# Kernel tuning notes

Measured on AMD Instinct MI355X. Metric: run time of the kernel, lower is better.

Reference implementation:

```python
import jax, jax.numpy as jnp
import numpy as np
from jax import lax

BN_EPS = 1e-5
K_TOP = 2


def _conv_bn_relu_pool(x, w, b, g, beta, mean, var):
    # x: [B,C,H,W], w: [O,I,3,3]; SAME conv -> eval BN -> ReLU -> 2x2 maxpool
    y = lax.conv_general_dilated(x, w, (1, 1), 'SAME',
                                 dimension_numbers=('NCHW', 'OIHW', 'NCHW'))
    y = y + b[None, :, None, None]
    inv = g / jnp.sqrt(var + BN_EPS)
    y = (y - mean[None, :, None, None]) * inv[None, :, None, None] + beta[None, :, None, None]
    y = jax.nn.relu(y)
    return lax.reduce_window(y, -jnp.inf, lax.max, (1, 1, 2, 2), (1, 1, 2, 2), 'VALID')


def setup_inputs() -> dict:
    key = jax.random.key(0)
    ks = jax.random.split(key, 12)
    B, F_DIM, H_DIM, OUT, E = 4096, 128, 64, 10, 8
    d = {}
    d['x'] = jax.random.normal(ks[0], (B, 3, 32, 32), dtype=jnp.float32)
    # conv stacks
    def conv_block(k, cin, cout, i):
        kk = jax.random.split(k, 2)
        d[f'conv{i}_w'] = jax.random.normal(kk[0], (cout, cin, 3, 3), dtype=jnp.float32) * (1.0 / np.sqrt(cin * 9))
        d[f'conv{i}_b'] = jnp.zeros((cout,), dtype=jnp.float32)
        d[f'bn{i}_g'] = jnp.ones((cout,), dtype=jnp.float32)
        d[f'bn{i}_b'] = jnp.zeros((cout,), dtype=jnp.float32)
        d[f'bn{i}_m'] = jax.random.normal(kk[1], (cout,), dtype=jnp.float32) * 0.1
        d[f'bn{i}_v'] = jnp.ones((cout,), dtype=jnp.float32)
    conv_block(ks[1], 3, 32, 1)
    conv_block(ks[2], 32, 64, 2)
    conv_block(ks[3], 64, 128, 3)
    # experts (stacked): MLPHead Linear(128,64) -> ReLU -> Linear(64,10)
    d['w1'] = jax.random.normal(ks[4], (E, F_DIM, H_DIM), dtype=jnp.float32) * (1.0 / np.sqrt(F_DIM))
    d['b1'] = jnp.zeros((E, H_DIM), dtype=jnp.float32)
    d['w2'] = jax.random.normal(ks[5], (E, H_DIM, OUT), dtype=jnp.float32) * (1.0 / np.sqrt(H_DIM))
    d['b2'] = jnp.zeros((E, OUT), dtype=jnp.float32)
    # top-k gate: Linear(128, 8)
    d['gate_w'] = jax.random.normal(ks[6], (F_DIM, E), dtype=jnp.float32) * (1.0 / np.sqrt(F_DIM))
    d['gate_b'] = jnp.zeros((E,), dtype=jnp.float32)
    return d


def reference(x, conv1_w, conv1_b, bn1_g, bn1_b, bn1_m, bn1_v,
              conv2_w, conv2_b, bn2_g, bn2_b, bn2_m, bn2_v,
              conv3_w, conv3_b, bn3_g, bn3_b, bn3_m, bn3_v,
              w1, b1, w2, b2, gate_w, gate_b):
    # Backbone: 3x32x32 -> 128 (eval-mode BN, dropout identity)
    h = _conv_bn_relu_pool(x, conv1_w, conv1_b, bn1_g, bn1_b, bn1_m, bn1_v)  # [B,32,16,16]
    h = _conv_bn_relu_pool(h, conv2_w, conv2_b, bn2_g, bn2_b, bn2_m, bn2_v)  # [B,64,8,8]
    h = _conv_bn_relu_pool(h, conv3_w, conv3_b, bn3_g, bn3_b, bn3_m, bn3_v)  # [B,128,4,4]
    feat = jnp.mean(h, axis=(2, 3))  # AdaptiveAvgPool2d(1) + Flatten -> [B,128]

    # Top-k gate: logits -> top-k -> softmax over selected -> scatter to [B,E]
    logits = feat @ gate_w + gate_b                     # [B,E]
    vals, idx = lax.top_k(logits, K_TOP)                # [B,k]
    wk = jax.nn.softmax(vals, axis=-1)                  # [B,k]
    B, E = logits.shape
    weights = jnp.zeros((B, E), dtype=logits.dtype)
    weights = weights.at[jnp.arange(B)[:, None], idx].set(wk)

    # Dense expert MLPs (as in source), gate-weighted sum
    he = jax.nn.relu(jnp.einsum('bf,efh->beh', feat, w1) + b1[None])  # [B,E,H]
    oe = jnp.einsum('beh,eho->beo', he, w2) + b2[None]                # [B,E,O]
    return jnp.einsum('be,beo->bo', weights, oe)                      # [B,O]
```

## Files before the change

### kernel.cpp

```cpp
#include <hip/hip_runtime.h>
#include <math.h>

typedef __attribute__((ext_vector_type(8))) short short8;
typedef __attribute__((ext_vector_type(4))) float f32x4;
#define MFMA __builtin_amdgcn_mfma_f32_16x16x32_bf16

#define BN_EPS 1e-5f

static const size_t W1C2_OFF = 0;
static const size_t W2C2_OFF = 1024;
static const size_t W3C2_OFF = 19456;
static const size_t B1_OFF   = 93184;
static const size_t B2_OFF   = 93216;
static const size_t B3_OFF   = 93280;

__device__ inline unsigned short rneb(float x) {
    unsigned u = __float_as_uint(x);
    return (unsigned short)((u + 0x7FFFu + ((u >> 16) & 1u)) >> 16);
}
__device__ inline float b2f(unsigned short h) {
    return __uint_as_float(((unsigned)h) << 16);
}

__global__ __launch_bounds__(256) void k_prep(
    const float* __restrict__ c1w, const float* __restrict__ c2w, const float* __restrict__ c3w,
    const float* __restrict__ c1b, const float* __restrict__ g1, const float* __restrict__ be1,
    const float* __restrict__ m1, const float* __restrict__ v1,
    const float* __restrict__ c2b, const float* __restrict__ g2, const float* __restrict__ be2,
    const float* __restrict__ m2, const float* __restrict__ v2,
    const float* __restrict__ c3b, const float* __restrict__ g3, const float* __restrict__ be3,
    const float* __restrict__ m3, const float* __restrict__ v3,
    unsigned short* __restrict__ w1c2, unsigned short* __restrict__ w2c2,
    unsigned short* __restrict__ w3c2,
    float* __restrict__ b1c, float* __restrict__ b2c, float* __restrict__ b3c)
{
    int i = blockIdx.x * 256 + threadIdx.x;
    if (i < 2048) {
        int e = i & 7, p = (i >> 3) & 1, kc = (i >> 4) & 3, ol = (i >> 6) & 15, n = i >> 10;
        int o = n * 16 + ol, k = kc * 8 + e;
        float s = g1[o] * rsqrtf(v1[o] + BN_EPS);
        float wv = (k < 27) ? c1w[o * 27 + k] * s : 0.f;
        unsigned short h = rneb(wv);
        w1c2[i] = p ? rneb(wv - b2f(h)) : h;
        return;
    }
    i -= 2048;
    if (i < 36864) {
        int e = i & 7, p = (i >> 3) & 1, kc = (i >> 4) & 3, ol = (i >> 6) & 15;
        int n = (i >> 10) & 3, tap = i >> 12;
        int o = n * 16 + ol, ci = kc * 8 + e;
        float s = g2[o] * rsqrtf(v2[o] + BN_EPS);
        float wv = c2w[o * 288 + ci * 9 + tap] * s;
        unsigned short h = rneb(wv);
        w2c2[i] = p ? rneb(wv - b2f(h)) : h;
        return;
    }
    i -= 36864;
    if (i < 147456) {
        int e = i & 7, p = (i >> 3) & 1, kc = (i >> 4) & 3, ol = (i >> 6) & 15;
        int nf = (i >> 10) & 7, s_ = (i >> 13) & 1, tap = i >> 14;
        int o = nf * 16 + ol, ci = s_ * 32 + kc * 8 + e;
        float sc = g3[o] * rsqrtf(v3[o] + BN_EPS);
        float wv = c3w[o * 576 + ci * 9 + tap] * sc;
        unsigned short h = rneb(wv);
        w3c2[i] = p ? rneb(wv - b2f(h)) : h;
        return;
    }
    i -= 147456;
    if (i < 32) { float s = g1[i]*rsqrtf(v1[i]+BN_EPS); b1c[i] = (c1b[i]-m1[i])*s + be1[i]; return; }
    i -= 32;
    if (i < 64) { float s = g2[i]*rsqrtf(v2[i]+BN_EPS); b2c[i] = (c2b[i]-m2[i])*s + be2[i]; return; }
    i -= 64;
    if (i < 128) { float s = g3[i]*rsqrtf(v3[i]+BN_EPS); b3c[i] = (c3b[i]-m3[i])*s + be3[i]; return; }
}

__global__ __launch_bounds__(512, 4) void k_fused(
    const float* __restrict__ x,
    const unsigned short* __restrict__ w1c2,
    const unsigned short* __restrict__ w2c2,
    const unsigned short* __restrict__ w3c2,
    const float* __restrict__ b1c, const float* __restrict__ b2c, const float* __restrict__ b3c,
    const float* __restrict__ w1e, const float* __restrict__ b1e,
    const float* __restrict__ w2e, const float* __restrict__ b2e,
    const float* __restrict__ gw, const float* __restrict__ gb,
    float* __restrict__ out)
{
    __shared__ __align__(16) unsigned short R1[20736];
    __shared__ __align__(16) unsigned short R2[6936];
    __shared__ float sFeat[128];
    __shared__ float sOut[2][10];

    const int b = blockIdx.x, t = threadIdx.x;
    const int lane = t & 63, w = t >> 6;
    const int l15 = lane & 15, lg = lane >> 4;

    for (int i = t; i < 10368; i += 512) ((int*)R1)[i] = 0;
    for (int i = t; i < 3468;  i += 512) ((int*)R2)[i] = 0;
    __syncthreads();
    {
        const float* xb = x + (size_t)b * 3072;
        for (int i = t; i < 3072; i += 512) {
            int ci = i >> 10, y = (i >> 5) & 31, xx = i & 31;
            float v = xb[i];
            unsigned short h = rneb(v), lo = rneb(v - b2f(h));
            int ei = ci * 1156 + (y + 1) * 34 + (xx + 1);
            R2[ei] = h; R2[3468 + ei] = lo;
        }
    }
    __syncthreads();

    {
        short8 b1h[2], b1l[2];
#pragma unroll
        for (int n = 0; n < 2; n++) {
            const short8* bp = (const short8*)(w1c2 + 16 * ((n * 16 + l15) * 4 + lg));
            b1h[n] = bp[0]; b1l[n] = bp[1];
        }
        int aoff[8];
#pragma unroll
        for (int e = 0; e < 8; e++) {
            int k = lg * 8 + e;
            if (k < 27) { int ci = k / 9; int tp = k - ci * 9; int dy = tp / 3, dx = tp - dy * 3;
                          aoff[e] = ci * 1156 + dy * 34 + dx; }
            else aoff[e] = 0;
        }
        float bia[2] = { b1c[l15], b1c[16 + l15] };
#pragma unroll 1
        for (int q = 0; q < 2; q++) {
            int m0 = 8 * w + 4 * q;
            f32x4 acc[4][2];
#pragma unroll
            for (int mi = 0; mi < 4; mi++)
#pragma unroll
                for (int n = 0; n < 2; n++) acc[mi][n] = (f32x4)0.f;
#pragma unroll
            for (int mi = 0; mi < 4; mi++) {
                int pos = 16 * (m0 + mi) + l15, py = pos >> 5, px = pos & 31;
                int base = py * 34 + px;
                short8 ah, al;
#pragma unroll
                for (int e = 0; e < 8; e++) {
                    ah[e] = (short)R2[base + aoff[e]];
                    al[e] = (short)R2[3468 + base + aoff[e]];
                }
#pragma unroll
                for (int n = 0; n < 2; n++) {
                    acc[mi][n] = MFMA(ah, b1h[n], acc[mi][n], 0, 0, 0);
                    acc[mi][n] = MFMA(ah, b1l[n], acc[mi][n], 0, 0, 0);
                    acc[mi][n] = MFMA(al, b1h[n], acc[mi][n], 0, 0, 0);
                }
            }
            int PY = 2 * w + q;
#pragma unroll
            for (int n = 0; n < 2; n++) {
                int o = n * 16 + l15;
#pragma unroll
                for (int h = 0; h < 2; h++)
#pragma unroll
                for (int jp = 0; jp < 2; jp++) {
                    float v00 = fmaxf(acc[h][n][2*jp]     + bia[n], 0.f);
                    float v01 = fmaxf(acc[h][n][2*jp + 1] + bia[n], 0.f);
                    float v10 = fmaxf(acc[h+2][n][2*jp]     + bia[n], 0.f);
                    float v11 = fmaxf(acc[h+2][n][2*jp + 1] + bia[n], 0.f);
                    float pm = fmaxf(fmaxf(v00, v01), fmaxf(v10, v11));
                    int PX = h * 8 + lg * 2 + jp;
                    unsigned short ph = rneb(pm), pl = rneb(pm - b2f(ph));
                    int ei = (((PY + 1) * 4 + (o >> 3)) * 18 + (PX + 1)) * 8 + (o & 7);
                    R1[ei] = ph; R1[10368 + ei] = pl;
                }
            }
        }
    }
    __syncthreads();

    {
        const int mh = w & 1, nn = w >> 1;
        f32x4 acc2[8];
#pragma unroll
        for (int mi = 0; mi < 8; mi++) acc2[mi] = (f32x4)0.f;
        const unsigned short* wb = w2c2 + ((size_t)(nn * 16 + l15) * 4 + lg) * 16;
        const int abase = (mh * 8) * 576 + lg * 144 + l15 * 8;
        short8 bhA, blA, bhB, blB;
#define LDB2(tp, BH, BL) { const short8* bp = (const short8*)(wb + (tp) * 4096); BH = bp[0]; BL = bp[1]; }
#define CMP2(tp, BH, BL) { int dy_ = (tp) / 3, dx_ = (tp) - 3 * dy_; \
        int roff_ = dy_ * 576 + dx_ * 8; \
        _Pragma("unroll") for (int mi = 0; mi < 8; mi++) { \
            int ea_ = abase + mi * 576 + roff_; \
            short8 ah_ = *(const short8*)(R1 + ea_); \
            short8 al_ = *(const short8*)(R1 + 10368 + ea_); \
            acc2[mi] = MFMA(ah_, BH, acc2[mi], 0, 0, 0); \
            acc2[mi] = MFMA(ah_, BL, acc2[mi], 0, 0, 0); \
            acc2[mi] = MFMA(al_, BH, acc2[mi], 0, 0, 0); } }
        LDB2(0, bhA, blA);
#pragma unroll 1
        for (int tp = 0; tp < 8; tp += 2) {
            LDB2(tp + 1, bhB, blB);
            CMP2(tp, bhA, blA);
            LDB2(tp + 2, bhA, blA);
            CMP2(tp + 1, bhB, blB);
        }
        CMP2(8, bhA, blA);
        __syncthreads();
        for (int i = t; i < 7040; i += 512) ((int*)R1)[i] = 0;
        __syncthreads();
        {
            int o = nn * 16 + l15;
            float bia = b2c[o];
#pragma unroll
            for (int mi2 = 0; mi2 < 4; mi2++) {
                int PY = mh * 4 + mi2;
#pragma unroll
                for (int jp = 0; jp < 2; jp++) {
                    float v00 = fmaxf(acc2[2*mi2][2*jp]     + bia, 0.f);
                    float v01 = fmaxf(acc2[2*mi2][2*jp + 1] + bia, 0.f);
                    float v10 = fmaxf(acc2[2*mi2+1][2*jp]     + bia, 0.f);
                    float v11 = fmaxf(acc2[2*mi2+1][2*jp + 1] + bia, 0.f);
                    float pm = fmaxf(fmaxf(v00, v01), fmaxf(v10, v11));
                    int PX = lg * 2 + jp;
                    unsigned short ph = rneb(pm), pl = rneb(pm - b2f(ph));
                    int ei = (((PY + 1) * 8 + (o >> 3)) * 11 + (PX + 1)) * 8 + (o & 7);
                    R1[ei] = ph; R1[7040 + ei] = pl;
                }
            }
        }
    }
    __syncthreads();

    {
        const int nf = w;
        f32x4 acc3[4];
#pragma unroll
        for (int mi = 0; mi < 4; mi++) acc3[mi] = (f32x4)0.f;
        const unsigned short* wb3 = w3c2 + ((size_t)(nf * 16 + l15) * 4 + lg) * 16;
        const int py0 = (l15 >> 3), px3 = l15 & 7;
        short8 bhA, blA, bhB, blB;
#define LDB3(ii, BH, BL) { const short8* bp = (const short8*)(wb3 + (ii) * 8192); BH = bp[0]; BL = bp[1]; }
#define CMP3(ii, BH, BL) { int tap_ = (ii) >> 1, s_ = (ii) & 1; \
        int dy_ = tap_ / 3, dx_ = tap_ - 3 * dy_; \
        int roff_ = dy_ * 704 + (s_ * 4 + lg) * 88 + dx_ * 8 + px3 * 8; \
        _Pragma("unroll") for (int mi = 0; mi < 4; mi++) { \
            int ea_ = (mi * 2 + py0) * 704 + roff_; \
            short8 ah_ = *(const short8*)(R1 + ea_); \
            short8 al_ = *(const short8*)(R1 + 7040 + ea_); \
            acc3[mi] = MFMA(ah_, BH, acc3[mi], 0, 0, 0); \
            acc3[mi] = MFMA(ah_, BL, acc3[mi], 0, 0, 0); \
            acc3[mi] = MFMA(al_, BH, acc3[mi], 0, 0, 0); } }
        LDB3(0, bhA, blA);
#pragma unroll 1
        for (int ii = 0; ii < 16; ii += 2) {
            LDB3(ii + 1, bhB, blB);
            CMP3(ii, bhA, blA);
            LDB3(ii + 2, bhA, blA);
            CMP3(ii + 1, bhB, blB);
        }
        LDB3(17, bhB, blB);
        CMP3(16, bhA, blA);
        CMP3(17, bhB, blB);
        {
            int o = nf * 16 + l15;
            float bia = b3c[o];
            float featsum = 0.f;
#pragma unroll
            for (int mi = 0; mi < 4; mi++) {
                float sumv = 0.f;
#pragma unroll
                for (int jp = 0; jp < 2; jp++) {
                    float v0 = fmaxf(acc3[mi][2*jp]     + bia, 0.f);
                    float v1 = fmaxf(acc3[mi][2*jp + 1] + bia, 0.f);
                    float vm = fmaxf(v0, v1);
                    vm = fmaxf(vm, __shfl_xor(vm, 32, 64));
                    sumv += vm;
                }
                sumv += __shfl_xor(sumv, 16, 64);
                featsum += sumv;
            }
            if (lane < 16) sFeat[nf * 16 + lane] = featsum * (1.0f / 16.0f);
        }
    }
    __syncthreads();

    if (w < 2) {
        float f0 = sFeat[lane], f1 = sFeat[64 + lane];
        float lgt[8];
#pragma unroll
        for (int e = 0; e < 8; e++) {
            float p = f0 * gw[lane * 8 + e] + f1 * gw[(64 + lane) * 8 + e];
#pragma unroll
            for (int s = 1; s < 64; s <<= 1) p += __shfl_xor(p, s, 64);
            lgt[e] = p + gb[e];
        }
        float v1m = -1e30f, v2m = -1e30f; int i1 = 0, i2 = 0;
#pragma unroll
        for (int e = 0; e < 8; e++) {
            float le = lgt[e];
            if (le > v1m) { v2m = v1m; i2 = i1; v1m = le; i1 = e; }
            else if (le > v2m) { v2m = le; i2 = e; }
        }
        float ex = expf(v2m - v1m);
        float wk = (w == 0) ? 1.f / (1.f + ex) : ex / (1.f + ex);
        int e = (w == 0) ? i1 : i2;
        const float* W1 = w1e + (size_t)e * 8192;
        float hj = b1e[e * 64 + lane];
#pragma unroll 8
        for (int k = 0; k < 128; k++) hj += sFeat[k] * W1[k * 64 + lane];
        hj = fmaxf(hj, 0.f);
        const float* W2 = w2e + (size_t)e * 640 + lane * 10;
#pragma unroll
        for (int o = 0; o < 10; o++) {
            float po = hj * W2[o];
#pragma unroll
            for (int s = 1; s < 64; s <<= 1) po += __shfl_xor(po, s, 64);
            if (lane == 0) sOut[w][o] = wk * (po + b2e[e * 10 + o]);
        }
    }
    __syncthreads();
    if (t < 10) out[(size_t)b * 10 + t] = sOut[0][t] + sOut[1][t];
}

extern "C" void kernel_launch(void* const* d_in, const int* in_sizes, int n_in,
                              void* d_out, int out_size, void* d_ws, size_t ws_size,
                              hipStream_t stream)
{
    const float* x   = (const float*)d_in[0];
    const float* c1w = (const float*)d_in[1];
    const float* c1b = (const float*)d_in[2];
    const float* g1  = (const float*)d_in[3];
    const float* be1 = (const float*)d_in[4];
    const float* m1  = (const float*)d_in[5];
    const float* v1  = (const float*)d_in[6];
    const float* c2w = (const float*)d_in[7];
    const float* c2b = (const float*)d_in[8];
    const float* g2  = (const float*)d_in[9];
    const float* be2 = (const float*)d_in[10];
    const float* m2  = (const float*)d_in[11];
    const float* v2  = (const float*)d_in[12];
    const float* c3w = (const float*)d_in[13];
    const float* c3b = (const float*)d_in[14];
    const float* g3  = (const float*)d_in[15];
    const float* be3 = (const float*)d_in[16];
    const float* m3  = (const float*)d_in[17];
    const float* v3  = (const float*)d_in[18];
    const float* w1e = (const float*)d_in[19];
    const float* b1e = (const float*)d_in[20];
    const float* w2e = (const float*)d_in[21];
    const float* b2e = (const float*)d_in[22];
    const float* gw  = (const float*)d_in[23];
    const float* gb  = (const float*)d_in[24];

    float* ws = (float*)d_ws;
    unsigned short* w1c2 = (unsigned short*)(ws + W1C2_OFF);
    unsigned short* w2c2 = (unsigned short*)(ws + W2C2_OFF);
    unsigned short* w3c2 = (unsigned short*)(ws + W3C2_OFF);
    float* b1c = ws + B1_OFF;
    float* b2c = ws + B2_OFF;
    float* b3c = ws + B3_OFF;

    k_prep<<<729, 256, 0, stream>>>(c1w, c2w, c3w,
                                    c1b, g1, be1, m1, v1,
                                    c2b, g2, be2, m2, v2,
                                    c3b, g3, be3, m3, v3,
                                    w1c2, w2c2, w3c2, b1c, b2c, b3c);
    k_fused<<<4096, 512, 0, stream>>>(x, w1c2, w2c2, w3c2, b1c, b2c, b3c,
                                      w1e, b1e, w2e, b2e, gw, gb, (float*)d_out);
}
```

Before: 303.6 us.

## Shrink LDS footprint, zero only halos, and split expert MLP across all waves

Replaces the padded split hi/lo input buffer with a packed unpadded 32-bit buffer that is bounds-checked at gather time, and zeroes only the halo borders of R1 instead of whole-buffer clears. This removes a barrier and the full clear passes. It also reuses the input buffer for feature and output scratch and raises the launch-bounds occupancy hint from 4 to 6. The first expert layer's 128-long reduction is split across all 8 waves through a partial-sum buffer. Risks: more address arithmetic and branches per gather, and register pressure from the higher occupancy target.

Result: slower. 318.6 us (+5.0%).

```diff
diff --git a/kernel.cpp b/kernel.cpp
--- a/kernel.cpp
+++ b/kernel.cpp
@@ -74,7 +74,7 @@
     if (i < 128) { float s = g3[i]*rsqrtf(v3[i]+BN_EPS); b3c[i] = (c3b[i]-m3[i])*s + be3[i]; return; }
 }
 
-__global__ __launch_bounds__(512, 4) void k_fused(
+__global__ __launch_bounds__(512, 6) void k_fused(
     const float* __restrict__ x,
     const unsigned short* __restrict__ w1c2,
     const unsigned short* __restrict__ w2c2,
@@ -86,25 +86,33 @@
     float* __restrict__ out)
 {
     __shared__ __align__(16) unsigned short R1[20736];
-    __shared__ __align__(16) unsigned short R2[6936];
-    __shared__ float sFeat[128];
-    __shared__ float sOut[2][10];
+    __shared__ __align__(16) unsigned int   R2x[3074];
+    float* sFeat = (float*)R2x;
+    float* sOutB = (float*)R2x + 128;
+    float* sPart = (float*)R2x + 160;
 
     const int b = blockIdx.x, t = threadIdx.x;
     const int lane = t & 63, w = t >> 6;
     const int l15 = lane & 15, lg = lane >> 4;
-
-    for (int i = t; i < 10368; i += 512) ((int*)R1)[i] = 0;
-    for (int i = t; i < 3468;  i += 512) ((int*)R2)[i] = 0;
-    __syncthreads();
+    const int4 z4 = {0, 0, 0, 0};
+
     {
         const float* xb = x + (size_t)b * 3072;
         for (int i = t; i < 3072; i += 512) {
-            int ci = i >> 10, y = (i >> 5) & 31, xx = i & 31;
             float v = xb[i];
-            unsigned short h = rneb(v), lo = rneb(v - b2f(h));
-            int ei = ci * 1156 + (y + 1) * 34 + (xx + 1);
-            R2[ei] = h; R2[3468 + ei] = lo;
+            unsigned short h = rneb(v);
+            unsigned short lo = rneb(v - b2f(h));
+            R2x[i] = ((unsigned)h << 16) | lo;
+        }
+        if (t == 0) R2x[3072] = 0;
+        for (int hh = t; hh < 272; hh += 512) {
+            int pr = hh >> 2, kc = hh & 3;
+            int py, px;
+            if (pr < 36) { py = (pr < 18) ? 0 : 17; px = (pr < 18) ? pr : pr - 18; }
+            else { int r = pr - 36; py = 1 + (r >> 1); px = (r & 1) ? 17 : 0; }
+            int ei = ((py * 4 + kc) * 18 + px) * 8;
+            *(int4*)(R1 + ei) = z4;
+            *(int4*)(R1 + 10368 + ei) = z4;
         }
     }
     __syncthreads();
@@ -116,13 +124,13 @@
             const short8* bp = (const short8*)(w1c2 + 16 * ((n * 16 + l15) * 4 + lg));
             b1h[n] = bp[0]; b1l[n] = bp[1];
         }
-        int aoff[8];
+        int dyE[8], dxE[8], cbE[8];
 #pragma unroll
         for (int e = 0; e < 8; e++) {
             int k = lg * 8 + e;
-            if (k < 27) { int ci = k / 9; int tp = k - ci * 9; int dy = tp / 3, dx = tp - dy * 3;
-                          aoff[e] = ci * 1156 + dy * 34 + dx; }
-            else aoff[e] = 0;
+            if (k < 27) { int ci = k / 9, tp = k - ci * 9;
+                          dyE[e] = tp / 3 - 1; dxE[e] = tp % 3 - 1; cbE[e] = ci << 10; }
+            else { dyE[e] = -1000; dxE[e] = 0; cbE[e] = 0; }
         }
         float bia[2] = { b1c[l15], b1c[16 + l15] };
 #pragma unroll 1
@@ -136,12 +144,15 @@
 #pragma unroll
             for (int mi = 0; mi < 4; mi++) {
                 int pos = 16 * (m0 + mi) + l15, py = pos >> 5, px = pos & 31;
-                int base = py * 34 + px;
                 short8 ah, al;
 #pragma unroll
                 for (int e = 0; e < 8; e++) {
-                    ah[e] = (short)R2[base + aoff[e]];
-                    al[e] = (short)R2[3468 + base + aoff[e]];
+                    int yy = py + dyE[e], xv = px + dxE[e];
+                    int idx = cbE[e] + (yy << 5) + xv;
+                    bool ok = ((unsigned)yy < 32u) && ((unsigned)xv < 32u);
+                    unsigned u = R2x[ok ? idx : 3072];
+                    ah[e] = (short)(u >> 16);
+                    al[e] = (short)(u & 0xFFFFu);
                 }
 #pragma unroll
                 for (int n = 0; n < 2; n++) {
@@ -201,8 +212,15 @@
         }
         CMP2(8, bhA, blA);
         __syncthreads();
-        for (int i = t; i < 7040; i += 512) ((int*)R1)[i] = 0;
-        __syncthreads();
+        for (int hh = t; hh < 288; hh += 512) {
+            int pr = hh >> 3, kc = hh & 7;
+            int py, px;
+            if (pr < 20) { py = (pr < 10) ? 0 : 9; px = (pr < 10) ? pr : pr - 10; }
+            else { int r = pr - 20; py = 1 + (r >> 1); px = (r & 1) ? 9 : 0; }
+            int ei = ((py * 8 + kc) * 11 + px) * 8;
+            *(int4*)(R1 + ei) = z4;
+            *(int4*)(R1 + 7040 + ei) = z4;
+        }
         {
             int o = nn * 16 + l15;
             float bia = b2c[o];
@@ -279,7 +297,9 @@
     }
     __syncthreads();
 
-    if (w < 2) {
+    int i1 = 0, i2 = 0;
+    float wk1 = 0.f, wk2 = 0.f;
+    {
         float f0 = sFeat[lane], f1 = sFeat[64 + lane];
         float lgt[8];
 #pragma unroll
@@ -289,7 +309,7 @@
             for (int s = 1; s < 64; s <<= 1) p += __shfl_xor(p, s, 64);
             lgt[e] = p + gb[e];
         }
-        float v1m = -1e30f, v2m = -1e30f; int i1 = 0, i2 = 0;
+        float v1m = -1e30f, v2m = -1e30f;
 #pragma unroll
         for (int e = 0; e < 8; e++) {
             float le = lgt[e];
@@ -297,12 +317,22 @@
             else if (le > v2m) { v2m = le; i2 = e; }
         }
         float ex = expf(v2m - v1m);
-        float wk = (w == 0) ? 1.f / (1.f + ex) : ex / (1.f + ex);
+        wk1 = 1.f / (1.f + ex); wk2 = ex / (1.f + ex);
+        int e = (w < 4) ? i1 : i2;
+        int k0 = (w & 3) * 32;
+        const float* W1 = w1e + (size_t)e * 8192 + (size_t)k0 * 64;
+        float hj = 0.f;
+#pragma unroll 8
+        for (int kk = 0; kk < 32; kk++) hj += sFeat[k0 + kk] * W1[kk * 64 + lane];
+        sPart[w * 64 + lane] = hj;
+    }
+    __syncthreads();
+    if (w < 2) {
         int e = (w == 0) ? i1 : i2;
-        const float* W1 = w1e + (size_t)e * 8192;
-        float hj = b1e[e * 64 + lane];
-#pragma unroll 8
-        for (int k = 0; k < 128; k++) hj += sFeat[k] * W1[k * 64 + lane];
+        float wk = (w == 0) ? wk1 : wk2;
+        float hj = b1e[e * 64 + lane]
+                 + sPart[(w * 4 + 0) * 64 + lane] + sPart[(w * 4 + 1) * 64 + lane]
+                 + sPart[(w * 4 + 2) * 64 + lane] + sPart[(w * 4 + 3) * 64 + lane];
         hj = fmaxf(hj, 0.f);
         const float* W2 = w2e + (size_t)e * 640 + lane * 10;
 #pragma unroll
@@ -310,11 +340,11 @@
             float po = hj * W2[o];
 #pragma unroll
             for (int s = 1; s < 64; s <<= 1) po += __shfl_xor(po, s, 64);
-            if (lane == 0) sOut[w][o] = wk * (po + b2e[e * 10 + o]);
-        }
-    }
-    __syncthreads();
-    if (t < 10) out[(size_t)b * 10 + t] = sOut[0][t] + sOut[1][t];
+            if (lane == 0) sOutB[w * 10 + o] = wk * (po + b2e[e * 10 + o]);
+        }
+    }
+    __syncthreads();
+    if (t < 10) out[(size_t)b * 10 + t] = sOutB[t] + sOutB[10 + t];
 }
 
 extern "C" void kernel_launch(void* const* d_in, const int* in_sizes, int n_in,
```
